# Performance work log

Measured on AMD Instinct MI355X. Metric: run time of the kernel, lower is better.

The kernel has to match this reference:

```python
import jax, jax.numpy as jnp
import numpy as np

COMMITMENT_COST = 0.25
NUM_EMBEDDINGS = 512
EMBEDDING_DIM = 64


def setup_inputs() -> dict:
    key = jax.random.key(0)
    k1, k2 = jax.random.split(key)
    inputs = jax.random.normal(k1, (32, EMBEDDING_DIM, 64, 64), dtype=jnp.float32)  # NCHW
    embedding_weight = jax.random.normal(k2, (NUM_EMBEDDINGS, EMBEDDING_DIM), dtype=jnp.float32)
    return {"inputs": inputs, "embedding_weight": embedding_weight}


def reference(inputs, embedding_weight):
    # NCHW -> NHWC, flatten to [N, D]
    x = jnp.transpose(inputs, (0, 2, 3, 1))  # [B,H,W,D]
    input_shape = x.shape
    flat = x.reshape(-1, EMBEDDING_DIM)  # [N, D]

    distances = (jnp.sum(flat * flat, axis=1, keepdims=True)
                 + jnp.sum(embedding_weight * embedding_weight, axis=1)
                 - 2.0 * jnp.matmul(flat, embedding_weight.T))

    encoding_indices = jnp.argmin(distances, axis=1)  # [N]
    encodings = jax.nn.one_hot(encoding_indices, NUM_EMBEDDINGS, dtype=jnp.float32)  # [N, K]

    # quantized lookup (== encodings @ embedding_weight)
    quantized = jnp.take(embedding_weight, encoding_indices, axis=0).reshape(input_shape)

    # commitment loss (eval path; EMA buffer updates are a training-time side effect)
    encoder_loss = jnp.mean((jax.lax.stop_gradient(quantized) - x) ** 2)
    loss = COMMITMENT_COST * encoder_loss

    # straight-through estimator
    quantized_st = x + jax.lax.stop_gradient(quantized - x)

    avg_probs = jnp.mean(encodings, axis=0)
    perplexity = jnp.exp(-jnp.sum(avg_probs * jnp.log(avg_probs + 1e-10)))

    return (loss, jnp.transpose(quantized_st, (0, 3, 1, 2)), perplexity, encodings)
```

## Files before the change

kernel.cpp:

```cpp
#include <hip/hip_runtime.h>
#include <math.h>

#define N_ROWS 131072
#define D 64
#define K 512
#define BLK 512
#define ROWS_PER_BLK 512
#define GRID (N_ROWS / ROWS_PER_BLK)
#define MARGIN 4e-3f


typedef __attribute__((ext_vector_type(8))) _Float16 f16x8;
typedef __attribute__((ext_vector_type(4))) float    f32x4;

#define MFMA(a, b, c) __builtin_amdgcn_mfma_f32_16x16x32_f16((a), (b), (c), 0, 0, 0)

#define OFF_EH   0
#define OFF_EL   65536
#define OFF_XH   0
#define OFF_XL   65536
#define OFF_E2   131072
#define OFF_IDX  133120
#define OFF_REF  135168
#define ARENA_SZ 137216

__device__ __forceinline__ unsigned pk2(_Float16 a, _Float16 b) {
    return (unsigned)__builtin_bit_cast(unsigned short, a) |
           ((unsigned)__builtin_bit_cast(unsigned short, b) << 16);
}

#define CT_ALL(M) M(0) M(1) M(2) M(3)
#define RT_ALL(M) M(0) M(1) M(2) M(3)

__global__ __launch_bounds__(BLK, 2) void vq_dist_kernel(
    const float* __restrict__ in,
    const float* __restrict__ emb,
    float* __restrict__ quant_out,
    float* __restrict__ enc_out)
{
    __shared__ __align__(16) char s_arena[ARENA_SZ];
    float* e2L    = (float*)(s_arena + OFF_E2);
    int*   s_idxL = (int*)(s_arena + OFF_IDX);
    int*   s_refL = (int*)(s_arena + OFF_REF);

    const int tid  = threadIdx.x;
    const int lane = tid & 63;
    const int w    = tid >> 6;
    const int fr   = lane & 15;
    const int fq   = lane >> 4;

    {
        const int nn = blockIdx.x * ROWS_PER_BLK + tid;
        const int bb = nn >> 12, hww = nn & 4095;
        const float* xp = in + (size_t)bb * 262144 + hww;
        char* xhW = s_arena + OFF_XH;
        char* xlW = s_arena + OFF_XL;
        const unsigned rbase = (unsigned)tid * 128u;
        const unsigned rxor  = (unsigned)((tid & 7) << 4);
        #pragma unroll
        for (int i = 0; i < 64; i += 2) {
            float f0 = xp[i * 4096];
            float f1 = xp[(i + 1) * 4096];
            _Float16 h0 = (_Float16)f0; _Float16 l0 = (_Float16)(f0 - (float)h0);
            _Float16 h1 = (_Float16)f1; _Float16 l1 = (_Float16)(f1 - (float)h1);
            unsigned off = rbase + (((unsigned)(i * 2)) ^ rxor);
            *(unsigned*)(xhW + off) = pk2(h0, h1);
            *(unsigned*)(xlW + off) = pk2(l0, l1);
        }
    }
    __syncthreads();

    const char* xb = s_arena;
    const int xr0 = w * 64 + fr;
#define LDX1(t, half) \
    *(const f16x8*)(xb + OFF_XH + (unsigned)(xr0 + t * 16) * 128u + \
        (((unsigned)(fq * 16 + half * 64)) ^ ((unsigned)(((xr0 + t * 16) & 7) << 4))))
#define LDX1L(t, half) \
    *(const f16x8*)(xb + OFF_XL + (unsigned)(xr0 + t * 16) * 128u + \
        (((unsigned)(fq * 16 + half * 64)) ^ ((unsigned)(((xr0 + t * 16) & 7) << 4))))
#define LDXF(t) \
    f16x8 xh##t##_0 = LDX1(t, 0); \
    f16x8 xh##t##_1 = LDX1(t, 1); \
    f16x8 xl##t##_0 = LDX1L(t, 0); \
    f16x8 xl##t##_1 = LDX1L(t, 1);
    RT_ALL(LDXF)
#undef LDXF
#undef LDX1
#undef LDX1L
    __syncthreads();

    {
        char* eb = s_arena;
        #pragma unroll
        for (int it = 0; it < 16; ++it) {
            int j = tid + it * 512;
            int c = j >> 4, q = j & 15;
            float4 e = ((const float4*)emb)[j];
            _Float16 h0 = (_Float16)e.x; _Float16 l0 = (_Float16)(e.x - (float)h0);
            _Float16 h1 = (_Float16)e.y; _Float16 l1 = (_Float16)(e.y - (float)h1);
            _Float16 h2 = (_Float16)e.z; _Float16 l2 = (_Float16)(e.z - (float)h2);
            _Float16 h3 = (_Float16)e.w; _Float16 l3 = (_Float16)(e.w - (float)h3);
            unsigned xr = (unsigned)((c & 7) << 4);
            unsigned base = (unsigned)(c * 128) + (((unsigned)(q * 8)) ^ xr);
            *(uint2*)(eb + OFF_EH + base) = make_uint2(pk2(h0, h1), pk2(h2, h3));
            *(uint2*)(eb + OFF_EL + base) = make_uint2(pk2(l0, l1), pk2(l2, l3));

            float p = e.x * e.x;
            p = fmaf(e.y, e.y, p);
            p = fmaf(e.z, e.z, p);
            p = fmaf(e.w, e.w, p);
            p += __shfl_xor(p, 1);
            p += __shfl_xor(p, 2);
            p += __shfl_xor(p, 4);
            p += __shfl_xor(p, 8);
            if (q == 0) e2L[c] = p;
        }
    }
    __syncthreads();

#define DECL(rt) \
    float s1_##rt = INFINITY, s2_##rt = INFINITY; \
    int   i1_##rt = 0, i2_##rt = 0;
    RT_ALL(DECL)
#undef DECL
#define UPD(rt, s, ki) { \
    bool lt1 = (s) < s1_##rt; bool lt2 = (s) < s2_##rt; \
    s2_##rt = lt1 ? s1_##rt : (lt2 ? (s) : s2_##rt); \
    i2_##rt = lt1 ? i1_##rt : (lt2 ? (ki) : i2_##rt); \
    s1_##rt = lt1 ? (s) : s1_##rt; \
    i1_##rt = lt1 ? (ki) : i1_##rt; }

    const char* ebase = s_arena;
    for (int cb = 0; cb < 8; ++cb) {
        const int cbBase = cb * 64 + fq * 4;

#define LDE2(ct) f32x4 e2q##ct = *(const f32x4*)(e2L + cb * 64 + ct * 16 + fq * 4);
        CT_ALL(LDE2)
#undef LDE2

#define LDE(ct) \
        const int c##ct = cb * 64 + ct * 16 + fr; \
        const char* rb##ct = ebase + c##ct * 128; \
        const unsigned xr##ct = (unsigned)((c##ct & 7) << 4); \
        f16x8 eh##ct##_0 = *(const f16x8*)(rb##ct + OFF_EH + (((unsigned)(fq*16 +  0)) ^ xr##ct)); \
        f16x8 eh##ct##_1 = *(const f16x8*)(rb##ct + OFF_EH + (((unsigned)(fq*16 + 64)) ^ xr##ct)); \
        f16x8 el##ct##_0 = *(const f16x8*)(rb##ct + OFF_EL + (((unsigned)(fq*16 +  0)) ^ xr##ct)); \
        f16x8 el##ct##_1 = *(const f16x8*)(rb##ct + OFF_EL + (((unsigned)(fq*16 + 64)) ^ xr##ct));
        CT_ALL(LDE)
#undef LDE

#define ACC1(rt, ct) \
        f32x4 a##rt##_##ct = {0.f, 0.f, 0.f, 0.f}; \
        a##rt##_##ct = MFMA(eh##ct##_0, xh##rt##_0, a##rt##_##ct); \
        a##rt##_##ct = MFMA(eh##ct##_1, xh##rt##_1, a##rt##_##ct); \
        a##rt##_##ct = MFMA(el##ct##_0, xh##rt##_0, a##rt##_##ct); \
        a##rt##_##ct = MFMA(el##ct##_1, xh##rt##_1, a##rt##_##ct); \
        a##rt##_##ct = MFMA(eh##ct##_0, xl##rt##_0, a##rt##_##ct); \
        a##rt##_##ct = MFMA(eh##ct##_1, xl##rt##_1, a##rt##_##ct);
#define ACC_CT(ct) ACC1(0, ct) ACC1(1, ct) ACC1(2, ct) ACC1(3, ct)
        CT_ALL(ACC_CT)
#undef ACC_CT
#undef ACC1

#define SCJ(rt, ct, j) { \
        float s = fmaf(-2.f, a##rt##_##ct[j], e2q##ct[j]); \
        int ki = cbBase + ct * 16 + j; \
        UPD(rt, s, ki) }
#define SC4(rt, ct) SCJ(rt, ct, 0) SCJ(rt, ct, 1) SCJ(rt, ct, 2) SCJ(rt, ct, 3)
#define SC_CT(ct) SC4(0, ct) SC4(1, ct) SC4(2, ct) SC4(3, ct)
        CT_ALL(SC_CT)
#undef SC_CT
#undef SC4
#undef SCJ
    }

#define MERGE(rt, off) { \
    float b1 = __shfl_xor(s1_##rt, off); int bi1 = __shfl_xor(i1_##rt, off); \
    float b2 = __shfl_xor(s2_##rt, off); int bi2 = __shfl_xor(i2_##rt, off); \
    bool bf = (b1 < s1_##rt) || (b1 == s1_##rt && bi1 < i1_##rt); \
    float c1 = bf ? b1 : s1_##rt; int ci1 = bf ? bi1 : i1_##rt; \
    float lw = bf ? s1_##rt : b1; int lwi = bf ? i1_##rt : bi1; \
    float d2 = bf ? b2 : s2_##rt; int di2 = bf ? bi2 : i2_##rt; \
    bool ds = (d2 < lw) || (d2 == lw && di2 < lwi); \
    s1_##rt = c1; i1_##rt = ci1; \
    s2_##rt = ds ? d2 : lw; i2_##rt = ds ? di2 : lwi; }
#define MERGE2(rt) MERGE(rt, 16) MERGE(rt, 32)
    RT_ALL(MERGE2)
#undef MERGE2
#undef MERGE

    if (fq == 0) {
#define WRT(rt) \
        s_idxL[w * 64 + rt * 16 + fr] = i1_##rt; \
        s_refL[w * 64 + rt * 16 + fr] = (s2_##rt - s1_##rt < MARGIN) ? i2_##rt : -1;
        RT_ALL(WRT)
#undef WRT
    }
#undef UPD

    {
        const int n = blockIdx.x * ROWS_PER_BLK + tid;
        const int b = n >> 12, hw = n & 4095;
        int i1 = s_idxL[tid];
        const int ir = s_refL[tid];
        if (ir >= 0) {
            const float* xin = in + (size_t)b * 262144 + hw;
            double dA = 0.0, dB = 0.0;
            const float* eA = emb + i1 * D;
            const float* eB = emb + ir * D;
            for (int d = 0; d < D; ++d) {
                double xv = (double)xin[d * 4096];
                double tA = xv - (double)eA[d]; dA = fma(tA, tA, dA);
                double tB = xv - (double)eB[d]; dB = fma(tB, tB, dB);
            }
            if (dB < dA || (dB == dA && ir < i1)) i1 = ir;
        }
        const float fbits = __int_as_float(i1);
        enc_out[(size_t)n * K] = fbits;
        quant_out[(size_t)b * 262144 + hw] = fbits;
    }
}

__global__ __launch_bounds__(256) void vq_out_kernel(
    const float* __restrict__ in,
    const float* __restrict__ emb,
    unsigned int* __restrict__ counts,
    unsigned long long* __restrict__ loss_acc,
    float* __restrict__ quant_out,
    float* __restrict__ enc)
{
    __shared__ unsigned int s_hist[K];
    __shared__ double s_red[256];
    const int tid = threadIdx.x;
    const int grp = blockIdx.x / 5;
    const int sub = blockIdx.x % 5;

    if (sub < 4) {
        const int eb   = grp * 4 + sub;
        const int wv   = tid >> 6;
        const int lane = tid & 63;
        const size_t row0 = (size_t)eb * 64 + (size_t)wv * 16;

        int idxs[16];
        #pragma unroll
        for (int i = 0; i < 16; ++i)
            idxs[i] = __float_as_int(enc[(row0 + i) * K]);

        const int c0 = lane * 4;
        #pragma unroll
        for (int i = 0; i < 16; ++i) {
            const int idx = idxs[i];
            float* rp = enc + (row0 + i) * K;
            f32x4 v0, v1;
            v0.x = (c0 + 0 == idx) ? 1.f : 0.f;
            v0.y = (c0 + 1 == idx) ? 1.f : 0.f;
            v0.z = (c0 + 2 == idx) ? 1.f : 0.f;
            v0.w = (c0 + 3 == idx) ? 1.f : 0.f;
            v1.x = (256 + c0 + 0 == idx) ? 1.f : 0.f;
            v1.y = (256 + c0 + 1 == idx) ? 1.f : 0.f;
            v1.z = (256 + c0 + 2 == idx) ? 1.f : 0.f;
            v1.w = (256 + c0 + 3 == idx) ? 1.f : 0.f;
            __builtin_nontemporal_store(v0, (f32x4*)(rp + c0));
            __builtin_nontemporal_store(v1, (f32x4*)(rp + 256 + c0));
        }
        return;
    }

    const int n = grp * 256 + tid;
    s_hist[tid] = 0u; s_hist[tid + 256] = 0u;
    __syncthreads();

    const int b = n >> 12, hw = n & 4095;
    const float* xin = in + (size_t)b * 262144 + hw;
    const int i1 = __float_as_int(quant_out[(size_t)b * 262144 + hw]);
    atomicAdd(&s_hist[i1], 1u);

    const float4* eq = (const float4*)(emb + (size_t)i1 * D);
    float* qout = quant_out + (size_t)b * 262144 + hw;
    float lsum = 0.f;
    #pragma unroll
    for (int i = 0; i < 16; ++i) {
        float4 q = eq[i];
        float x0 = xin[(4 * i + 0) * 4096], x1 = xin[(4 * i + 1) * 4096];
        float x2 = xin[(4 * i + 2) * 4096], x3 = xin[(4 * i + 3) * 4096];
        float d0 = q.x - x0; lsum = fmaf(d0, d0, lsum);
        float d1 = q.y - x1; lsum = fmaf(d1, d1, lsum);
        float d2 = q.z - x2; lsum = fmaf(d2, d2, lsum);
        float d3 = q.w - x3; lsum = fmaf(d3, d3, lsum);
        __builtin_nontemporal_store(q.x, &qout[(4 * i + 0) * 4096]);
        __builtin_nontemporal_store(q.y, &qout[(4 * i + 1) * 4096]);
        __builtin_nontemporal_store(q.z, &qout[(4 * i + 2) * 4096]);
        __builtin_nontemporal_store(q.w, &qout[(4 * i + 3) * 4096]);
    }

    s_red[tid] = (double)lsum;
    __syncthreads();
    for (int s = 128; s > 0; s >>= 1) {
        if (tid < s) s_red[tid] += s_red[tid + s];
        __syncthreads();
    }
    if (tid == 0) {
        unsigned long long q =
            (unsigned long long)(long long)llrint(s_red[0] * 1073741824.0);
        atomicAdd(loss_acc, q);
    }
    {
        unsigned int c0h = s_hist[tid];
        if (c0h) atomicAdd(&counts[tid], c0h);
        unsigned int c1h = s_hist[tid + 256];
        if (c1h) atomicAdd(&counts[tid + 256], c1h);
    }
}

__global__ __launch_bounds__(512) void vq_final_kernel(
    const unsigned int* __restrict__ counts,
    const unsigned long long* __restrict__ loss_acc,
    float* __restrict__ out_loss,
    float* __restrict__ out_perp)
{
    __shared__ double sp[512];
    int t = threadIdx.x;
    double p = (double)counts[t] / (double)N_ROWS;
    sp[t] = p * log(p + 1e-10);
    __syncthreads();
    for (int s = 256; s > 0; s >>= 1) {
        if (t < s) sp[t] += sp[t + s];
        __syncthreads();
    }
    if (t == 0) {
        double ls = (double)(long long)(*loss_acc) * (1.0 / 1073741824.0);
        *out_loss = (float)(0.25 * ls / 8388608.0);
        *out_perp = (float)exp(-sp[0]);
    }
}

extern "C" void kernel_launch(void* const* d_in, const int* in_sizes, int n_in,
                              void* d_out, int out_size, void* d_ws, size_t ws_size,
                              hipStream_t stream) {
    const float* in  = (const float*)d_in[0];
    const float* emb = (const float*)d_in[1];
    float* out = (float*)d_out;

    unsigned int* counts = (unsigned int*)d_ws;
    unsigned long long* loss_acc = (unsigned long long*)((char*)d_ws + 2048);

    hipMemsetAsync(d_ws, 0, 2056, stream);
    vq_dist_kernel<<<GRID, BLK, 0, stream>>>(in, emb, out + 1, out + 8388610);
    vq_out_kernel<<<2560, 256, 0, stream>>>(in, emb, counts, loss_acc,
                                            out + 1, out + 8388610);
    vq_final_kernel<<<1, 512, 0, stream>>>(counts, loss_acc, out, out + 8388609);
}
```

Baseline: 123.4 us.

## Fold loss and histogram into distance kernel using argmin distance plus norm

The commitment-loss and code-usage histogram move from the output kernel into the distance kernel. Each row's loss is taken as the minimum distance plus the row's squared norm, accumulated while the input is staged, or as the exact fp64 distance when a refinement check runs. This removes the second full read of the input tensor and the per-block reductions from the output kernel. It adds LDS atomics and a 512-wide fp64 reduction to the distance kernel, and the loss now depends on the accuracy of the split-fp16 MFMA distance.

```diff
diff --git a/kernel.cpp b/kernel.cpp
--- a/kernel.cpp
+++ b/kernel.cpp
@@ -20,9 +20,9 @@
 #define OFF_XH   0
 #define OFF_XL   65536
 #define OFF_E2   131072
-#define OFF_IDX  133120
-#define OFF_REF  135168
-#define ARENA_SZ 137216
+#define OFF_HIST 133120
+#define OFF_RED  135168
+#define ARENA_SZ 139264
 
 __device__ __forceinline__ unsigned pk2(_Float16 a, _Float16 b) {
     return (unsigned)__builtin_bit_cast(unsigned short, a) |
@@ -35,13 +35,15 @@
 __global__ __launch_bounds__(BLK, 2) void vq_dist_kernel(
     const float* __restrict__ in,
     const float* __restrict__ emb,
+    unsigned int* __restrict__ counts,
+    unsigned long long* __restrict__ loss_acc,
     float* __restrict__ quant_out,
     float* __restrict__ enc_out)
 {
     __shared__ __align__(16) char s_arena[ARENA_SZ];
-    float* e2L    = (float*)(s_arena + OFF_E2);
-    int*   s_idxL = (int*)(s_arena + OFF_IDX);
-    int*   s_refL = (int*)(s_arena + OFF_REF);
+    float*        e2L    = (float*)(s_arena + OFF_E2);
+    unsigned int* s_hstL = (unsigned int*)(s_arena + OFF_HIST);
+    double*       s_redL = (double*)(s_arena + OFF_RED);
 
     const int tid  = threadIdx.x;
     const int lane = tid & 63;
@@ -49,6 +51,7 @@
     const int fr   = lane & 15;
     const int fq   = lane >> 4;
 
+    float x2 = 0.f;
     {
         const int nn = blockIdx.x * ROWS_PER_BLK + tid;
         const int bb = nn >> 12, hww = nn & 4095;
@@ -61,6 +64,8 @@
         for (int i = 0; i < 64; i += 2) {
             float f0 = xp[i * 4096];
             float f1 = xp[(i + 1) * 4096];
+            x2 = fmaf(f0, f0, x2);
+            x2 = fmaf(f1, f1, x2);
             _Float16 h0 = (_Float16)f0; _Float16 l0 = (_Float16)(f0 - (float)h0);
             _Float16 h1 = (_Float16)f1; _Float16 l1 = (_Float16)(f1 - (float)h1);
             unsigned off = rbase + (((unsigned)(i * 2)) ^ rxor);
@@ -115,6 +120,7 @@
             p += __shfl_xor(p, 8);
             if (q == 0) e2L[c] = p;
         }
+        s_hstL[tid] = 0u;
     }
     __syncthreads();
 
@@ -188,49 +194,65 @@
     RT_ALL(MERGE2)
 #undef MERGE2
 #undef MERGE
-
-    if (fq == 0) {
-#define WRT(rt) \
-        s_idxL[w * 64 + rt * 16 + fr] = i1_##rt; \
-        s_refL[w * 64 + rt * 16 + fr] = (s2_##rt - s1_##rt < MARGIN) ? i2_##rt : -1;
-        RT_ALL(WRT)
-#undef WRT
-    }
 #undef UPD
 
     {
         const int n = blockIdx.x * ROWS_PER_BLK + tid;
         const int b = n >> 12, hw = n & 4095;
-        int i1 = s_idxL[tid];
-        const int ir = s_refL[tid];
-        if (ir >= 0) {
+
+#define REFV(rt) ((s2_##rt - s1_##rt < MARGIN) ? i2_##rt : -1)
+        const int rt0 = lane >> 4;
+        float s1own = (rt0 == 0) ? s1_0 : (rt0 == 1) ? s1_1 : (rt0 == 2) ? s1_2 : s1_3;
+        int   i1own = (rt0 == 0) ? i1_0 : (rt0 == 1) ? i1_1 : (rt0 == 2) ? i1_2 : i1_3;
+        int   irown = (rt0 == 0) ? REFV(0) : (rt0 == 1) ? REFV(1) : (rt0 == 2) ? REFV(2) : REFV(3);
+#undef REFV
+
+        double lrow;
+        if (irown >= 0) {
             const float* xin = in + (size_t)b * 262144 + hw;
             double dA = 0.0, dB = 0.0;
-            const float* eA = emb + i1 * D;
-            const float* eB = emb + ir * D;
+            const float* eA = emb + i1own * D;
+            const float* eB = emb + irown * D;
             for (int d = 0; d < D; ++d) {
                 double xv = (double)xin[d * 4096];
                 double tA = xv - (double)eA[d]; dA = fma(tA, tA, dA);
                 double tB = xv - (double)eB[d]; dB = fma(tB, tB, dB);
             }
-            if (dB < dA || (dB == dA && ir < i1)) i1 = ir;
+            if (dB < dA || (dB == dA && irown < i1own)) { i1own = irown; lrow = dB; }
+            else lrow = dA;
+        } else {
+            lrow = (double)s1own + (double)x2;
         }
-        const float fbits = __int_as_float(i1);
+
+        atomicAdd(&s_hstL[i1own], 1u);
+        s_redL[tid] = lrow;
+
+        const float fbits = __int_as_float(i1own);
         enc_out[(size_t)n * K] = fbits;
         quant_out[(size_t)b * 262144 + hw] = fbits;
     }
+
+    __syncthreads();
+    for (int s = BLK / 2; s > 0; s >>= 1) {
+        if (tid < s) s_redL[tid] += s_redL[tid + s];
+        __syncthreads();
+    }
+    if (tid == 0) {
+        unsigned long long q =
+            (unsigned long long)(long long)llrint(s_redL[0] * 1073741824.0);
+        atomicAdd(loss_acc, q);
+    }
+    {
+        unsigned int c = s_hstL[tid];
+        if (c) atomicAdd(&counts[tid], c);
+    }
 }
 
 __global__ __launch_bounds__(256) void vq_out_kernel(
-    const float* __restrict__ in,
     const float* __restrict__ emb,
-    unsigned int* __restrict__ counts,
-    unsigned long long* __restrict__ loss_acc,
     float* __restrict__ quant_out,
     float* __restrict__ enc)
 {
-    __shared__ unsigned int s_hist[K];
-    __shared__ double s_red[256];
     const int tid = threadIdx.x;
     const int grp = blockIdx.x / 5;
     const int sub = blockIdx.x % 5;
@@ -267,48 +289,17 @@
     }
 
     const int n = grp * 256 + tid;
-    s_hist[tid] = 0u; s_hist[tid + 256] = 0u;
-    __syncthreads();
-
     const int b = n >> 12, hw = n & 4095;
-    const float* xin = in + (size_t)b * 262144 + hw;
-    const int i1 = __float_as_int(quant_out[(size_t)b * 262144 + hw]);
-    atomicAdd(&s_hist[i1], 1u);
-
+    float* qout = quant_out + (size_t)b * 262144 + hw;
+    const int i1 = __float_as_int(qout[0]);
     const float4* eq = (const float4*)(emb + (size_t)i1 * D);
-    float* qout = quant_out + (size_t)b * 262144 + hw;
-    float lsum = 0.f;
     #pragma unroll
     for (int i = 0; i < 16; ++i) {
         float4 q = eq[i];
-        float x0 = xin[(4 * i + 0) * 4096], x1 = xin[(4 * i + 1) * 4096];
-        float x2 = xin[(4 * i + 2) * 4096], x3 = xin[(4 * i + 3) * 4096];
-        float d0 = q.x - x0; lsum = fmaf(d0, d0, lsum);
-        float d1 = q.y - x1; lsum = fmaf(d1, d1, lsum);
-        float d2 = q.z - x2; lsum = fmaf(d2, d2, lsum);
-        float d3 = q.w - x3; lsum = fmaf(d3, d3, lsum);
         __builtin_nontemporal_store(q.x, &qout[(4 * i + 0) * 4096]);
         __builtin_nontemporal_store(q.y, &qout[(4 * i + 1) * 4096]);
         __builtin_nontemporal_store(q.z, &qout[(4 * i + 2) * 4096]);
         __builtin_nontemporal_store(q.w, &qout[(4 * i + 3) * 4096]);
-    }
-
-    s_red[tid] = (double)lsum;
-    __syncthreads();
-    for (int s = 128; s > 0; s >>= 1) {
-        if (tid < s) s_red[tid] += s_red[tid + s];
-        __syncthreads();
-    }
-    if (tid == 0) {
-        unsigned long long q =
-            (unsigned long long)(long long)llrint(s_red[0] * 1073741824.0);
-        atomicAdd(loss_acc, q);
-    }
-    {
-        unsigned int c0h = s_hist[tid];
-        if (c0h) atomicAdd(&counts[tid], c0h);
-        unsigned int c1h = s_hist[tid + 256];
-        if (c1h) atomicAdd(&counts[tid + 256], c1h);
     }
 }
 
@@ -345,8 +336,8 @@
     unsigned long long* loss_acc = (unsigned long long*)((char*)d_ws + 2048);
 
     hipMemsetAsync(d_ws, 0, 2056, stream);
-    vq_dist_kernel<<<GRID, BLK, 0, stream>>>(in, emb, out + 1, out + 8388610);
-    vq_out_kernel<<<2560, 256, 0, stream>>>(in, emb, counts, loss_acc,
-                                            out + 1, out + 8388610);
+    vq_dist_kernel<<<GRID, BLK, 0, stream>>>(in, emb, counts, loss_acc,
+                                             out + 1, out + 8388610);
+    vq_out_kernel<<<2560, 256, 0, stream>>>(emb, out + 1, out + 8388610);
     vq_final_kernel<<<1, 512, 0, stream>>>(counts, loss_acc, out, out + 8388609);
 }
```

After: 122.2 us. No clear change (-1.0%).
